# Optimization experiments

Hardware: AMD Instinct MI355X
Metric: run time of the kernel (lower is better)

The kernel has to match this reference:

```python
import jax, jax.numpy as jnp
import numpy as np

B, S, H, E, V = 4, 256, 1024, 1024, 50257
PAD = 0
DOM = 0.9   # skipLayersDominance
EPS = 1e-5  # LayerNorm eps (torch default)


def setup_inputs() -> dict:
    key = jax.random.key(0)
    ks = jax.random.split(key, 6)
    emb = jax.random.normal(ks[0], (V, E), jnp.float32) * 0.02
    emb = emb.at[PAD].set(0.0)  # padding_idx row zeroed like nn.Embedding
    labels = jax.random.randint(ks[1], (B, S), 0, V)
    W_in = jax.random.normal(ks[2], (E, H), jnp.float32) * (1.0 / np.sqrt(E))
    b_in = jnp.zeros((H,), jnp.float32)
    # Conv1d(2H, H, kernel_size=1, groups=H) weight -> [H, 2] (per-head pair mix)
    W_sani = jax.random.normal(ks[3], (H, 2), jnp.float32) * (1.0 / np.sqrt(2.0))
    b_sani = jnp.zeros((H,), jnp.float32)
    ln_w = jnp.ones((H,), jnp.float32)
    ln_b = jnp.zeros((H,), jnp.float32)
    W_out = jax.random.normal(ks[4], (H, E), jnp.float32) * (1.0 / np.sqrt(H))
    b_out = jnp.zeros((E,), jnp.float32)
    return dict(labels=labels, emb=emb, W_in=W_in, b_in=b_in, W_sani=W_sani,
                b_sani=b_sani, ln_w=ln_w, ln_b=ln_b, W_out=W_out, b_out=b_out)


def _layernorm(x, w, b):
    mu = x.mean(-1, keepdims=True)
    var = x.var(-1, keepdims=True)
    return (x - mu) * jax.lax.rsqrt(var + EPS) * w + b


def _forward(labels, emb, W_in, b_in, W_sani, b_sani, ln_w, ln_b, W_out, b_out):
    x = emb[labels]                                # [B,S,E] inputsEmbeddings
    h = jax.nn.relu(x @ W_in + b_in)               # [B,S,H] inputState
    pos = jnp.arange(S)

    def step(hidden, L):
        # positions <= L are replaced by blank (zeros) per the torch cat logic
        mask = (pos > L)[None, :, None]
        shifted = jnp.concatenate([jnp.zeros_like(hidden[:, :1]), hidden[:, :-1]], axis=1)
        prev = jnp.where(mask, shifted, 0.0)       # hidden[t-1] for t>L else 0
        curr = jnp.where(mask, hidden, 0.0)        # hidden[t]   for t>L else 0
        # torch stack(dim=1)+reshape(B, 2H, 1) == concat(prev, curr) on features;
        # grouped conv (groups=H, 2 ch/group, k=1): out[g] = W[g,0]*cat[2g] + W[g,1]*cat[2g+1] + b[g]
        pair = jnp.concatenate([prev, curr], axis=-1).reshape(B, S, H, 2)
        out = jax.nn.relu(jnp.einsum('bshc,hc->bsh', pair, W_sani) + b_sani)
        out = out * (1.0 - DOM) + hidden           # skipLayers: + sequentialInputState
        out = _layernorm(out, ln_w, ln_b)           # skipLayersNorm
        return out, None

    h, _ = jax.lax.scan(jax.checkpoint(step), h, jnp.arange(S))
    y = jax.nn.relu(h @ W_out + b_out)             # [B,S,E]
    # torch CrossEntropyLoss with float (soft) targets: classes along dim=1 (S)
    logp = jax.nn.log_softmax(y, axis=1)
    loss = -(x * logp).sum(axis=1).mean()
    return loss


def reference(labels, emb, W_in, b_in, W_sani, b_sani, ln_w, ln_b, W_out, b_out):
    return _forward(labels, emb, W_in, b_in, W_sani, b_sani, ln_w, ln_b, W_out, b_out)
```

## Files before the change

### kernel.cpp

```cpp
#include <hip/hip_runtime.h>
#include <cstdint>

#define H_DIM 1024
#define S_LEN 256
#define B_SZ  4
#define T_ROWS 8
#define NBLK_SCAN 128
#define GDEPTH 8
#define DOMC ((float)(1.0 - 0.9))
#define EPS_LN 1e-5f

typedef float v2f __attribute__((ext_vector_type(2)));

template <int CTRL, int RMASK, bool BC>
__device__ __forceinline__ float dpp_term(float x) {
    return __int_as_float(__builtin_amdgcn_update_dpp(
        0, __float_as_int(x), CTRL, RMASK, 0xf, BC));
}
__device__ __forceinline__ float wave_reduce_sum(float x) {
    x += dpp_term<0x111, 0xf, true>(x);
    x += dpp_term<0x112, 0xf, true>(x);
    x += dpp_term<0x114, 0xf, true>(x);
    x += dpp_term<0x118, 0xf, true>(x);
    x += dpp_term<0x142, 0xa, false>(x);
    x += dpp_term<0x143, 0xc, false>(x);
    return __int_as_float(__builtin_amdgcn_readlane(__float_as_int(x), 63));
}

__device__ __forceinline__ int llc_load_int(const int* p) {
    int v;
    asm volatile("global_load_dword %0, %1, off sc0 sc1\n\ts_waitcnt vmcnt(0)"
                 : "=v"(v) : "v"(p) : "memory");
    return v;
}
__device__ __forceinline__ void llc_store_int(int* p, int v) {
    asm volatile("global_store_dword %0, %1, off sc0 sc1" :: "v"(p), "v"(v)
                 : "memory");
}
__device__ __forceinline__ void llc_store_row_nowait(float* base, const float* h) {
    asm volatile(
        "global_store_dword %16, %0, off sc0 sc1\n\t"
        "global_store_dword %16, %1, off offset:256 sc0 sc1\n\t"
        "global_store_dword %16, %2, off offset:512 sc0 sc1\n\t"
        "global_store_dword %16, %3, off offset:768 sc0 sc1\n\t"
        "global_store_dword %16, %4, off offset:1024 sc0 sc1\n\t"
        "global_store_dword %16, %5, off offset:1280 sc0 sc1\n\t"
        "global_store_dword %16, %6, off offset:1536 sc0 sc1\n\t"
        "global_store_dword %16, %7, off offset:1792 sc0 sc1\n\t"
        "global_store_dword %16, %8, off offset:2048 sc0 sc1\n\t"
        "global_store_dword %16, %9, off offset:2304 sc0 sc1\n\t"
        "global_store_dword %16, %10, off offset:2560 sc0 sc1\n\t"
        "global_store_dword %16, %11, off offset:2816 sc0 sc1\n\t"
        "global_store_dword %16, %12, off offset:3072 sc0 sc1\n\t"
        "global_store_dword %16, %13, off offset:3328 sc0 sc1\n\t"
        "global_store_dword %16, %14, off offset:3584 sc0 sc1\n\t"
        "global_store_dword %16, %15, off offset:3840 sc0 sc1"
        :: "v"(h[0]), "v"(h[1]), "v"(h[2]), "v"(h[3]),
           "v"(h[4]), "v"(h[5]), "v"(h[6]), "v"(h[7]),
           "v"(h[8]), "v"(h[9]), "v"(h[10]), "v"(h[11]),
           "v"(h[12]), "v"(h[13]), "v"(h[14]), "v"(h[15]), "v"(base)
        : "memory");
}
__device__ __forceinline__ void llc_publish(float* dbase, int* flagp,
                                            int flagval, const float* h) {
    asm volatile(
        "s_waitcnt vmcnt(0)\n\t"
        "global_store_dword %17, %18, off sc0 sc1\n\t"
        "global_store_dword %16, %0, off sc0 sc1\n\t"
        "global_store_dword %16, %1, off offset:256 sc0 sc1\n\t"
        "global_store_dword %16, %2, off offset:512 sc0 sc1\n\t"
        "global_store_dword %16, %3, off offset:768 sc0 sc1\n\t"
        "global_store_dword %16, %4, off offset:1024 sc0 sc1\n\t"
        "global_store_dword %16, %5, off offset:1280 sc0 sc1\n\t"
        "global_store_dword %16, %6, off offset:1536 sc0 sc1\n\t"
        "global_store_dword %16, %7, off offset:1792 sc0 sc1\n\t"
        "global_store_dword %16, %8, off offset:2048 sc0 sc1\n\t"
        "global_store_dword %16, %9, off offset:2304 sc0 sc1\n\t"
        "global_store_dword %16, %10, off offset:2560 sc0 sc1\n\t"
        "global_store_dword %16, %11, off offset:2816 sc0 sc1\n\t"
        "global_store_dword %16, %12, off offset:3072 sc0 sc1\n\t"
        "global_store_dword %16, %13, off offset:3328 sc0 sc1\n\t"
        "global_store_dword %16, %14, off offset:3584 sc0 sc1\n\t"
        "global_store_dword %16, %15, off offset:3840 sc0 sc1"
        :: "v"(h[0]), "v"(h[1]), "v"(h[2]), "v"(h[3]),
           "v"(h[4]), "v"(h[5]), "v"(h[6]), "v"(h[7]),
           "v"(h[8]), "v"(h[9]), "v"(h[10]), "v"(h[11]),
           "v"(h[12]), "v"(h[13]), "v"(h[14]), "v"(h[15]),
           "v"(dbase), "v"(flagp), "v"(flagval)
        : "memory");
}
__device__ __forceinline__ void llc_release(int* flagp, int flagval) {
    asm volatile("s_waitcnt vmcnt(0)\n\t"
                 "global_store_dword %0, %1, off sc0 sc1"
                 :: "v"(flagp), "v"(flagval) : "memory");
}
__device__ __forceinline__ void llc_load_pairs(
    const float* base, v2f& p0, v2f& p1, v2f& p2, v2f& p3,
    v2f& p4, v2f& p5, v2f& p6, v2f& p7) {
    asm volatile(
        "global_load_dwordx2 %0, %8, off sc0 sc1\n\t"
        "global_load_dwordx2 %1, %8, off offset:512 sc0 sc1\n\t"
        "global_load_dwordx2 %2, %8, off offset:1024 sc0 sc1\n\t"
        "global_load_dwordx2 %3, %8, off offset:1536 sc0 sc1\n\t"
        "global_load_dwordx2 %4, %8, off offset:2048 sc0 sc1\n\t"
        "global_load_dwordx2 %5, %8, off offset:2560 sc0 sc1\n\t"
        "global_load_dwordx2 %6, %8, off offset:3072 sc0 sc1\n\t"
        "global_load_dwordx2 %7, %8, off offset:3584 sc0 sc1\n\t"
        "s_waitcnt vmcnt(0)"
        : "=&v"(p0), "=&v"(p1), "=&v"(p2), "=&v"(p3),
          "=&v"(p4), "=&v"(p5), "=&v"(p6), "=&v"(p7)
        : "v"(base)
        : "memory");
}

template <bool GATHER>
__global__ __launch_bounds__(256) void gemm_relu_kernel(
    const float* __restrict__ A, const int* __restrict__ labels,
    const float* __restrict__ emb, const float* __restrict__ W,
    const float* __restrict__ bias, float* __restrict__ out)
{
    __shared__ float As[16][68];
    __shared__ float Bs[16][64];
    __shared__ int   lab[64];

    const int tid = threadIdx.x;
    const int bx = blockIdx.x & 15;
    const int by = blockIdx.x >> 4;
    const int m0 = by * 64, n0 = bx * 64;

    if (GATHER && tid < 64) lab[tid] = labels[m0 + tid];
    __syncthreads();

    const int tx = tid & 15, ty = tid >> 4;
    const int mload = tid >> 2;
    const int kq    = (tid & 3) * 4;
    const int kb    = tid >> 4;
    const int nb    = (tid & 15) * 4;

    float acc[4][4] = {};

    for (int k0 = 0; k0 < 1024; k0 += 16) {
        const float* arow;
        if (GATHER) arow = emb + (size_t)lab[mload] * 1024 + k0 + kq;
        else        arow = A   + (size_t)(m0 + mload) * 1024 + k0 + kq;
        float4 a4 = *(const float4*)arow;
        As[kq + 0][mload] = a4.x;
        As[kq + 1][mload] = a4.y;
        As[kq + 2][mload] = a4.z;
        As[kq + 3][mload] = a4.w;

        float4 b4 = *(const float4*)&W[(size_t)(k0 + kb) * 1024 + n0 + nb];
        *(float4*)&Bs[kb][nb] = b4;
        __syncthreads();

#pragma unroll
        for (int kk = 0; kk < 16; ++kk) {
            float a_[4];
#pragma unroll
            for (int i = 0; i < 4; ++i) a_[i] = As[kk][ty * 4 + i];
            float4 bv = *(const float4*)&Bs[kk][tx * 4];
            float b_[4] = {bv.x, bv.y, bv.z, bv.w};
#pragma unroll
            for (int i = 0; i < 4; ++i)
#pragma unroll
                for (int j = 0; j < 4; ++j)
                    acc[i][j] = fmaf(a_[i], b_[j], acc[i][j]);
        }
        __syncthreads();
    }

    float bias4[4];
#pragma unroll
    for (int j = 0; j < 4; ++j) bias4[j] = bias[n0 + tx * 4 + j];
#pragma unroll
    for (int i = 0; i < 4; ++i) {
        float4 o;
        o.x = fmaxf(acc[i][0] + bias4[0], 0.f);
        o.y = fmaxf(acc[i][1] + bias4[1], 0.f);
        o.z = fmaxf(acc[i][2] + bias4[2], 0.f);
        o.w = fmaxf(acc[i][3] + bias4[3], 0.f);
        *(float4*)&out[(size_t)(m0 + ty * 4 + i) * 1024 + n0 + tx * 4] = o;
    }
}

__global__ __launch_bounds__(256) void scan_init_kernel(
    int* __restrict__ prodG, int* __restrict__ consG)
{
    const int tid = threadIdx.x;
    if (tid < NBLK_SCAN) { prodG[tid * 16] = -2; consG[tid * 16] = -2; }
}

__global__ __launch_bounds__(512, 1) void scan_kernel(
    const float* __restrict__ h0, float* __restrict__ hf,
    const float* __restrict__ Wsani, const float* __restrict__ bsani,
    const float* __restrict__ lnw, const float* __restrict__ lnb,
    float* __restrict__ gbuf, int* __restrict__ prodG, int* __restrict__ consG)
{
    __shared__ float ring[7][2][H_DIM];
    __shared__ float self7[H_DIM];
    __shared__ int prodL[8], consL[8];

    const int tid = threadIdx.x, w = tid >> 6, l = tid & 63;
    const int Bb = blockIdx.x;
    const int b = Bb >> 5, p = Bb & 31;
    const int t = T_ROWS * p + w;
    const int row = b * S_LEN + t;
    const int leftB = Bb - 1, rightB = Bb + 1;
    const bool hasR = (p < 31);

    float w0c[16], w1c[16], bsc[16], lwc[16], lbc[16], hv[16];
#pragma unroll
    for (int i = 0; i < 16; ++i) {
        int h = l + 64 * i;
        w0c[i] = Wsani[2 * h]; w1c[i] = Wsani[2 * h + 1];
        bsc[i] = bsani[h]; lwc[i] = lnw[h]; lbc[i] = lnb[h];
        hv[i] = h0[(size_t)row * H_DIM + h];
    }

    if (tid < 8) { prodL[tid] = -2; consL[tid] = -2; }
    __syncthreads();

    if (w < 7) {
#pragma unroll
        for (int i = 0; i < 16; ++i) ring[w][1][l + 64 * i] = hv[i];
        __threadfence_block();
        if (l == 0) ((volatile int*)prodL)[w] = -1;
    } else {
        if (hasR)
            llc_store_row_nowait(gbuf + ((size_t)Bb * GDEPTH + 7) * H_DIM + l, hv);
#pragma unroll
        for (int i = 0; i < 16; ++i) self7[l + 64 * i] = hv[i];
    }

    const float inv1024 = 1.f / 1024.f;
    int consGcache = -2;
    float vv[16];

    for (int L = 0; L < S_LEN; ++L) {
        const bool active = (L < t);
        if (active) {
            v2f pv[8], cv[8];
            if (w == 0) {
                const int* fp = prodG + leftB * 16;
                int f = llc_load_int(fp);
                while (f < L - 1) { __builtin_amdgcn_s_sleep(1); f = llc_load_int(fp); }
                const float* src =
                    gbuf + ((size_t)leftB * GDEPTH + ((L - 1) & 7)) * H_DIM + 2 * l;
                llc_load_pairs(src, pv[0], pv[1], pv[2], pv[3],
                                    pv[4], pv[5], pv[6], pv[7]);
                llc_store_int(consG + Bb * 16, L - 1);
                const float* srcc = &ring[0][(L - 1) & 1][0];
#pragma unroll
                for (int j = 0; j < 8; ++j)
                    cv[j] = *(const v2f*)&srcc[2 * l + 128 * j];
            } else {
                int spin = 0;
                while (((volatile int*)prodL)[w - 1] < L - 1)
                    { if (++spin > 8) __builtin_amdgcn_s_sleep(1); }
                const float* srcp = &ring[w - 1][(L - 1) & 1][0];
#pragma unroll
                for (int j = 0; j < 8; ++j)
                    pv[j] = *(const v2f*)&srcp[2 * l + 128 * j];
                const float* srcc = (w < 7) ? &ring[w][(L - 1) & 1][0] : &self7[0];
#pragma unroll
                for (int j = 0; j < 8; ++j)
                    cv[j] = *(const v2f*)&srcc[2 * l + 128 * j];
                if (l == 0) ((volatile int*)consL)[w] = L - 1;
            }
#pragma unroll
            for (int i = 0; i < 8; ++i) {
                float s = fmaf(pv[i].x, w0c[i], fmaf(pv[i].y, w1c[i], bsc[i]));
                s = fmaxf(s, 0.f);
                vv[i] = fmaf(DOMC, s, hv[i]);
            }
#pragma unroll
            for (int i = 8; i < 16; ++i) {
                float s = fmaf(cv[i - 8].x, w0c[i],
                               fmaf(cv[i - 8].y, w1c[i], bsc[i]));
                s = fmaxf(s, 0.f);
                vv[i] = fmaf(DOMC, s, hv[i]);
            }
        } else {
#pragma unroll
            for (int i = 0; i < 16; ++i) {
                float s = fmaxf(bsc[i], 0.f);
                vv[i] = fmaf(DOMC, s, hv[i]);
            }
        }
        float sum = 0.f, ss = 0.f;
#pragma unroll
        for (int i = 0; i < 16; ++i) { sum += vv[i]; ss = fmaf(vv[i], vv[i], ss); }
        sum = wave_reduce_sum(sum); ss = wave_reduce_sum(ss);
        const float mu = sum * inv1024;
        const float var = fmaf(-mu, mu, ss * inv1024);
        const float r = 1.f / sqrtf(var + EPS_LN);
#pragma unroll
        for (int i = 0; i < 16; ++i)
            hv[i] = fmaf((vv[i] - mu) * r, lwc[i], lbc[i]);

        if (active) {
            if (w < 7) {
                if (L >= 1) {
                    int spin = 0;
                    while (((volatile int*)consL)[w + 1] < L - 2)
                        { if (++spin > 8) __builtin_amdgcn_s_sleep(1); }
                }
#pragma unroll
                for (int i = 0; i < 16; ++i) ring[w][L & 1][l + 64 * i] = hv[i];
                __threadfence_block();
                if (l == 0) ((volatile int*)prodL)[w] = L;
            } else {
                if (hasR) {
                    if (L >= 7 && consGcache < L - GDEPTH) {
                        int c = llc_load_int(consG + rightB * 16);
                        while (c < L - GDEPTH) {
                            __builtin_amdgcn_s_sleep(1);
                            c = llc_load_int(consG + rightB * 16);
                        }
                        consGcache = c;
                    }
                    llc_publish(gbuf + ((size_t)Bb * GDEPTH + (L & 7)) * H_DIM + l,
                                prodG + Bb * 16, L - 1, hv);
                }
#pragma unroll
                for (int i = 0; i < 16; ++i) self7[l + 64 * i] = hv[i];
            }
        } else if (w == 7 && hasR && L == t) {
            llc_release(prodG + Bb * 16, t - 1);
        }
    }
#pragma unroll
    for (int i = 0; i < 16; ++i)
        hf[(size_t)row * H_DIM + l + 64 * i] = hv[i];
}

__global__ __launch_bounds__(256) void lse_kernel(
    const float* __restrict__ y, float* __restrict__ lse)
{
    const int b = blockIdx.x >> 4, et = blockIdx.x & 15;
    const int col = threadIdx.x & 63, rg = threadIdx.x >> 6;
    const int e = et * 64 + col;
    const float* yb = y + (size_t)b * S_LEN * H_DIM + e;
    float m = -INFINITY, s = 0.f;
    for (int r = rg; r < S_LEN; r += 4) {
        float v = yb[(size_t)r * H_DIM];
        float mn = fmaxf(m, v);
        s = fmaf(s, expf(m - mn), expf(v - mn));
        m = mn;
    }
    __shared__ float sm[4][64], sp[4][64];
    sm[rg][col] = m; sp[rg][col] = s;
    __syncthreads();
    if (threadIdx.x < 64) {
        const int c = threadIdx.x;
        float M = fmaxf(fmaxf(sm[0][c], sm[1][c]), fmaxf(sm[2][c], sm[3][c]));
        float S = sp[0][c] * expf(sm[0][c] - M) + sp[1][c] * expf(sm[1][c] - M)
                + sp[2][c] * expf(sm[2][c] - M) + sp[3][c] * expf(sm[3][c] - M);
        lse[b * H_DIM + et * 64 + c] = M + logf(S);
    }
}

__global__ __launch_bounds__(256) void loss_row_kernel(
    const float* __restrict__ y, const int* __restrict__ labels,
    const float* __restrict__ emb, const float* __restrict__ lse,
    float* __restrict__ partials)
{
    const int bs = blockIdx.x;
    const int b = bs >> 8;
    const int lab = labels[bs];
    const float* yr = y + (size_t)bs * H_DIM;
    const float* er = emb + (size_t)lab * H_DIM;
    const float* lr = lse + b * H_DIM;
    float acc = 0.f;
#pragma unroll
    for (int i = 0; i < 4; ++i) {
        int e = threadIdx.x + 256 * i;
        acc = fmaf(er[e], yr[e] - lr[e], acc);
    }
    acc = wave_reduce_sum(acc);
    __shared__ float wsum[4];
    if ((threadIdx.x & 63) == 0) wsum[threadIdx.x >> 6] = acc;
    __syncthreads();
    if (threadIdx.x == 0)
        partials[bs] = (wsum[0] + wsum[1]) + (wsum[2] + wsum[3]);
}

__global__ __launch_bounds__(256) void loss_final_kernel(
    const float* __restrict__ partials, float* __restrict__ out)
{
    const int tid = threadIdx.x;
    float a = 0.f;
#pragma unroll
    for (int j = 0; j < 4; ++j) a += partials[tid + 256 * j];
    a = wave_reduce_sum(a);
    __shared__ float wsum[4];
    if ((tid & 63) == 0) wsum[tid >> 6] = a;
    __syncthreads();
    if (tid == 0)
        out[0] = -((wsum[0] + wsum[1]) + (wsum[2] + wsum[3])) * (1.f / 4096.f);
}

extern "C" void kernel_launch(void* const* d_in, const int* in_sizes, int n_in,
                              void* d_out, int out_size, void* d_ws, size_t ws_size,
                              hipStream_t stream)
{
    const int*   labels = (const int*)  d_in[0];
    const float* emb    = (const float*)d_in[1];
    const float* W_in   = (const float*)d_in[2];
    const float* b_in   = (const float*)d_in[3];
    const float* W_sani = (const float*)d_in[4];
    const float* b_sani = (const float*)d_in[5];
    const float* ln_w   = (const float*)d_in[6];
    const float* ln_b   = (const float*)d_in[7];
    const float* W_out  = (const float*)d_in[8];
    const float* b_out  = (const float*)d_in[9];
    float* out = (float*)d_out;

    float* ws = (float*)d_ws;
    float* h0       = ws;
    float* hf       = ws + (1 << 20);
    float* yb       = ws + 2 * (1 << 20);
    float* gbuf     = ws + 3 * (1 << 20);
    float* lse      = ws + 4 * (1 << 20);
    float* partials = lse + 4096;
    int*   prodG    = (int*)(partials + 1024);
    int*   consG    = prodG + NBLK_SCAN * 16;

    gemm_relu_kernel<true><<<dim3(256), dim3(256), 0, stream>>>(
        nullptr, labels, emb, W_in, b_in, h0);
    scan_init_kernel<<<dim3(1), dim3(256), 0, stream>>>(prodG, consG);
    {
        const float* a_h0 = h0; float* a_hf = hf;
        const float* a_ws = W_sani; const float* a_bs = b_sani;
        const float* a_lw = ln_w;   const float* a_lb = ln_b;
        float* a_gb = gbuf; int* a_pf = prodG; int* a_cf = consG;
        void* args[] = { (void*)&a_h0, (void*)&a_hf, (void*)&a_ws, (void*)&a_bs,
                         (void*)&a_lw, (void*)&a_lb, (void*)&a_gb,
                         (void*)&a_pf, (void*)&a_cf };
        hipLaunchCooperativeKernel((const void*)scan_kernel,
                                   dim3(NBLK_SCAN), dim3(512), args, 0, stream);
    }
    gemm_relu_kernel<false><<<dim3(256), dim3(256), 0, stream>>>(
        hf, nullptr, emb, W_out, b_out, yb);
    lse_kernel<<<dim3(64), dim3(256), 0, stream>>>(yb, lse);
    loss_row_kernel<<<dim3(1024), dim3(256), 0, stream>>>(
        yb, labels, emb, lse, partials);
    loss_final_kernel<<<dim3(1), dim3(256), 0, stream>>>(partials, out);
}
```

Measured before the change: 803.4 us.

## Pipeline cross-block scan handoff with LDS DMA prefetch, deeper ring, lag-2 publish

The cross-block handoff in the sequential scan is reworked. The ring in global memory is doubled to 16 slots. The publisher's flag now lags by two steps, so it no longer waits for all prior stores to drain. The consumer wave prefetches the next slot straight into LDS with global_load_lds, and the self row for wave 7 is now built from registers with lane shuffles instead of an LDS round-trip. Separately, the GEMM kernel gains a one-stage register prefetch of the next k-tile, and the flag stride is widened to 32 ints. These changes target latency on the serial critical path, but they make the synchronization protocol harder to get right.

```diff
diff --git a/kernel.cpp b/kernel.cpp
--- a/kernel.cpp
+++ b/kernel.cpp
@@ -3,10 +3,8 @@
 
 #define H_DIM 1024
 #define S_LEN 256
-#define B_SZ  4
-#define T_ROWS 8
 #define NBLK_SCAN 128
-#define GDEPTH 8
+#define GDEPTH 16
 #define DOMC ((float)(1.0 - 0.9))
 #define EPS_LN 1e-5f
 
@@ -61,10 +59,10 @@
            "v"(h[12]), "v"(h[13]), "v"(h[14]), "v"(h[15]), "v"(base)
         : "memory");
 }
-__device__ __forceinline__ void llc_publish(float* dbase, int* flagp,
-                                            int flagval, const float* h) {
+__device__ __forceinline__ void llc_publish_lag2(float* dbase, int* flagp,
+                                                 int flagval, const float* h) {
     asm volatile(
-        "s_waitcnt vmcnt(0)\n\t"
+        "s_waitcnt vmcnt(16)\n\t"
         "global_store_dword %17, %18, off sc0 sc1\n\t"
         "global_store_dword %16, %0, off sc0 sc1\n\t"
         "global_store_dword %16, %1, off offset:256 sc0 sc1\n\t"
@@ -94,23 +92,28 @@
                  "global_store_dword %0, %1, off sc0 sc1"
                  :: "v"(flagp), "v"(flagval) : "memory");
 }
-__device__ __forceinline__ void llc_load_pairs(
-    const float* base, v2f& p0, v2f& p1, v2f& p2, v2f& p3,
-    v2f& p4, v2f& p5, v2f& p6, v2f& p7) {
-    asm volatile(
-        "global_load_dwordx2 %0, %8, off sc0 sc1\n\t"
-        "global_load_dwordx2 %1, %8, off offset:512 sc0 sc1\n\t"
-        "global_load_dwordx2 %2, %8, off offset:1024 sc0 sc1\n\t"
-        "global_load_dwordx2 %3, %8, off offset:1536 sc0 sc1\n\t"
-        "global_load_dwordx2 %4, %8, off offset:2048 sc0 sc1\n\t"
-        "global_load_dwordx2 %5, %8, off offset:2560 sc0 sc1\n\t"
-        "global_load_dwordx2 %6, %8, off offset:3072 sc0 sc1\n\t"
-        "global_load_dwordx2 %7, %8, off offset:3584 sc0 sc1\n\t"
-        "s_waitcnt vmcnt(0)"
-        : "=&v"(p0), "=&v"(p1), "=&v"(p2), "=&v"(p3),
-          "=&v"(p4), "=&v"(p5), "=&v"(p6), "=&v"(p7)
-        : "v"(base)
-        : "memory");
+
+__device__ __forceinline__ void dma_slot(const float* gslot, float* stg, int l) {
+#pragma unroll
+    for (int c = 0; c < 4; ++c)
+        __builtin_amdgcn_global_load_lds(
+            (const __attribute__((address_space(1))) uint32_t*)(gslot + c * 256 + l * 4),
+            (__attribute__((address_space(3))) uint32_t*)(stg + c * 256),
+            16, 0, 0x11);
+}
+
+__device__ __forceinline__ void make_pairs(const float* hv, v2f* c7, int l) {
+    const int s0 = (2 * l) & 63, s1 = (2 * l + 1) & 63;
+    const bool hi = (l >= 32);
+#pragma unroll
+    for (int j = 0; j < 8; ++j) {
+        float x0 = __shfl(hv[2 * j], s0, 64);
+        float x1 = __shfl(hv[2 * j + 1], s0, 64);
+        float y0 = __shfl(hv[2 * j], s1, 64);
+        float y1 = __shfl(hv[2 * j + 1], s1, 64);
+        c7[j].x = hi ? x1 : x0;
+        c7[j].y = hi ? y1 : y0;
+    }
 }
 
 template <bool GATHER>
@@ -137,21 +140,28 @@
     const int kb    = tid >> 4;
     const int nb    = (tid & 15) * 4;
 
+    const float* aBase;
+    if (GATHER) aBase = emb + (size_t)lab[mload] * 1024 + kq;
+    else        aBase = A   + (size_t)(m0 + mload) * 1024 + kq;
+    const float* bBase = W + (size_t)kb * 1024 + n0 + nb;
+
+    float4 a_pre = *(const float4*)aBase;
+    float4 b_pre = *(const float4*)bBase;
+
     float acc[4][4] = {};
 
     for (int k0 = 0; k0 < 1024; k0 += 16) {
-        const float* arow;
-        if (GATHER) arow = emb + (size_t)lab[mload] * 1024 + k0 + kq;
-        else        arow = A   + (size_t)(m0 + mload) * 1024 + k0 + kq;
-        float4 a4 = *(const float4*)arow;
-        As[kq + 0][mload] = a4.x;
-        As[kq + 1][mload] = a4.y;
-        As[kq + 2][mload] = a4.z;
-        As[kq + 3][mload] = a4.w;
-
-        float4 b4 = *(const float4*)&W[(size_t)(k0 + kb) * 1024 + n0 + nb];
-        *(float4*)&Bs[kb][nb] = b4;
+        As[kq + 0][mload] = a_pre.x;
+        As[kq + 1][mload] = a_pre.y;
+        As[kq + 2][mload] = a_pre.z;
+        As[kq + 3][mload] = a_pre.w;
+        *(float4*)&Bs[kb][nb] = b_pre;
         __syncthreads();
+
+        if (k0 + 16 < 1024) {
+            a_pre = *(const float4*)(aBase + k0 + 16);
+            b_pre = *(const float4*)(bBase + (size_t)(k0 + 16) * 1024);
+        }
 
 #pragma unroll
         for (int kk = 0; kk < 16; ++kk) {
@@ -187,7 +197,7 @@
     int* __restrict__ prodG, int* __restrict__ consG)
 {
     const int tid = threadIdx.x;
-    if (tid < NBLK_SCAN) { prodG[tid * 16] = -2; consG[tid * 16] = -2; }
+    if (tid < NBLK_SCAN) { prodG[tid * 32] = -2; consG[tid * 32] = -2; }
 }
 
 __global__ __launch_bounds__(512, 1) void scan_kernel(
@@ -197,16 +207,16 @@
     float* __restrict__ gbuf, int* __restrict__ prodG, int* __restrict__ consG)
 {
     __shared__ float ring[7][2][H_DIM];
-    __shared__ float self7[H_DIM];
+    __shared__ float stg[H_DIM];
     __shared__ int prodL[8], consL[8];
 
     const int tid = threadIdx.x, w = tid >> 6, l = tid & 63;
     const int Bb = blockIdx.x;
     const int b = Bb >> 5, p = Bb & 31;
-    const int t = T_ROWS * p + w;
+    const int t = 8 * p + w;
     const int row = b * S_LEN + t;
+    const bool hasR = (p < 31);
     const int leftB = Bb - 1, rightB = Bb + 1;
-    const bool hasR = (p < 31);
 
     float w0c[16], w1c[16], bsc[16], lwc[16], lbc[16], hv[16];
 #pragma unroll
@@ -220,6 +230,7 @@
     if (tid < 8) { prodL[tid] = -2; consL[tid] = -2; }
     __syncthreads();
 
+    v2f c7[8];
     if (w < 7) {
 #pragma unroll
         for (int i = 0; i < 16; ++i) ring[w][1][l + 64 * i] = hv[i];
@@ -227,13 +238,13 @@
         if (l == 0) ((volatile int*)prodL)[w] = -1;
     } else {
         if (hasR)
-            llc_store_row_nowait(gbuf + ((size_t)Bb * GDEPTH + 7) * H_DIM + l, hv);
-#pragma unroll
-        for (int i = 0; i < 16; ++i) self7[l + 64 * i] = hv[i];
+            llc_store_row_nowait(
+                gbuf + ((size_t)Bb * GDEPTH + (GDEPTH - 1)) * H_DIM + l, hv);
+        make_pairs(hv, c7, l);
     }
 
     const float inv1024 = 1.f / 1024.f;
-    int consGcache = -2;
+    int F = -2, pfL = -3, consCache = -2;
     float vv[16];
 
     for (int L = 0; L < S_LEN; ++L) {
@@ -241,18 +252,31 @@
         if (active) {
             v2f pv[8], cv[8];
             if (w == 0) {
-                const int* fp = prodG + leftB * 16;
-                int f = llc_load_int(fp);
-                while (f < L - 1) { __builtin_amdgcn_s_sleep(1); f = llc_load_int(fp); }
-                const float* src =
-                    gbuf + ((size_t)leftB * GDEPTH + ((L - 1) & 7)) * H_DIM + 2 * l;
-                llc_load_pairs(src, pv[0], pv[1], pv[2], pv[3],
-                                    pv[4], pv[5], pv[6], pv[7]);
-                llc_store_int(consG + Bb * 16, L - 1);
-                const float* srcc = &ring[0][(L - 1) & 1][0];
+                const int* fp = prodG + leftB * 32;
+                if (pfL != L - 1) {
+                    while (F < L - 1) {
+                        F = llc_load_int(fp);
+                        if (F < L - 1) __builtin_amdgcn_s_sleep(1);
+                    }
+                    dma_slot(gbuf + ((size_t)leftB * GDEPTH +
+                                     ((L - 1) & (GDEPTH - 1))) * H_DIM, stg, l);
+                    pfL = L - 1;
+                }
+                asm volatile("s_waitcnt vmcnt(0)" ::: "memory");
 #pragma unroll
                 for (int j = 0; j < 8; ++j)
-                    cv[j] = *(const v2f*)&srcc[2 * l + 128 * j];
+                    pv[j] = *(const v2f*)&stg[2 * l + 128 * j];
+#pragma unroll
+                for (int j = 0; j < 8; ++j)
+                    cv[j] = *(const v2f*)&ring[0][(L - 1) & 1][2 * l + 128 * j];
+                if (F < L) F = llc_load_int(fp);
+                if (F >= L && L < t - 1) {
+                    asm volatile("s_waitcnt lgkmcnt(0)" ::: "memory");
+                    dma_slot(gbuf + ((size_t)leftB * GDEPTH +
+                                     (L & (GDEPTH - 1))) * H_DIM, stg, l);
+                    pfL = L;
+                }
+                llc_store_int(consG + Bb * 32, L);
             } else {
                 int spin = 0;
                 while (((volatile int*)prodL)[w - 1] < L - 1)
@@ -261,10 +285,15 @@
 #pragma unroll
                 for (int j = 0; j < 8; ++j)
                     pv[j] = *(const v2f*)&srcp[2 * l + 128 * j];
-                const float* srcc = (w < 7) ? &ring[w][(L - 1) & 1][0] : &self7[0];
-#pragma unroll
-                for (int j = 0; j < 8; ++j)
-                    cv[j] = *(const v2f*)&srcc[2 * l + 128 * j];
+                if (w < 7) {
+                    const float* srcc = &ring[w][(L - 1) & 1][0];
+#pragma unroll
+                    for (int j = 0; j < 8; ++j)
+                        cv[j] = *(const v2f*)&srcc[2 * l + 128 * j];
+                } else {
+#pragma unroll
+                    for (int j = 0; j < 8; ++j) cv[j] = c7[j];
+                }
                 if (l == 0) ((volatile int*)consL)[w] = L - 1;
             }
 #pragma unroll
@@ -311,22 +340,22 @@
                 if (l == 0) ((volatile int*)prodL)[w] = L;
             } else {
                 if (hasR) {
-                    if (L >= 7 && consGcache < L - GDEPTH) {
-                        int c = llc_load_int(consG + rightB * 16);
-                        while (c < L - GDEPTH) {
+                    if (consCache < L - (GDEPTH - 3)) {
+                        int c = llc_load_int(consG + rightB * 32);
+                        while (c < L - (GDEPTH - 1)) {
                             __builtin_amdgcn_s_sleep(1);
-                            c = llc_load_int(consG + rightB * 16);
+                            c = llc_load_int(consG + rightB * 32);
                         }
-                        consGcache = c;
+                        consCache = c;
                     }
-                    llc_publish(gbuf + ((size_t)Bb * GDEPTH + (L & 7)) * H_DIM + l,
-                                prodG + Bb * 16, L - 1, hv);
+                    llc_publish_lag2(
+                        gbuf + ((size_t)Bb * GDEPTH + (L & (GDEPTH - 1))) * H_DIM + l,
+                        prodG + Bb * 32, L - 2, hv);
                 }
-#pragma unroll
-                for (int i = 0; i < 16; ++i) self7[l + 64 * i] = hv[i];
+                if (L + 1 < t) make_pairs(hv, c7, l);
             }
         } else if (w == 7 && hasR && L == t) {
-            llc_release(prodG + Bb * 16, t - 1);
+            llc_release(prodG + Bb * 32, t - 1);
         }
     }
 #pragma unroll
@@ -421,10 +450,10 @@
     float* hf       = ws + (1 << 20);
     float* yb       = ws + 2 * (1 << 20);
     float* gbuf     = ws + 3 * (1 << 20);
-    float* lse      = ws + 4 * (1 << 20);
+    float* lse      = ws + 5 * (1 << 20);
     float* partials = lse + 4096;
     int*   prodG    = (int*)(partials + 1024);
-    int*   consG    = prodG + NBLK_SCAN * 16;
+    int*   consG    = prodG + NBLK_SCAN * 32;
 
     gemm_relu_kernel<true><<<dim3(256), dim3(256), 0, stream>>>(
         nullptr, labels, emb, W_in, b_in, h0);
```

Result: faster. 756.8 us (-5.8%).
